# Kernel optimization log

Hardware: AMD Instinct MI355X
Metric: run time of the kernel (lower is better)

The kernel has to match this reference:

```python
import jax, jax.numpy as jnp
import numpy as np

B, S, H = 1, 2048, 4608
NH, NKV, HD = 36, 4, 128
GROUP = NH // NKV  # 9
ROPE_THETA = 100000.0
SLIDING_WINDOW = 1024


def _rope_tables(seq_len, head_dim):
    inv_freq = 1.0 / (ROPE_THETA ** (jnp.arange(0, head_dim, 2, dtype=jnp.float32) / head_dim))
    ang = jnp.arange(seq_len, dtype=jnp.float32)[:, None] * inv_freq[None, :]  # [S, HD/2]
    emb = jnp.concatenate([ang, ang], axis=-1)  # [S, HD]
    return jnp.cos(emb), jnp.sin(emb)


def setup_inputs() -> dict:
    key = jax.random.key(0)
    ks = jax.random.split(key, 10)
    std = 0.02
    cos_table, sin_table = _rope_tables(S, HD)
    return {
        "hidden_states": jax.random.normal(ks[0], (B, S, H), jnp.float32),
        "position_ids": jnp.broadcast_to(jnp.arange(S, dtype=jnp.int64)[None, :], (B, S)),
        "cos_table": cos_table,
        "sin_table": sin_table,
        "q_w": jax.random.normal(ks[1], (NH * HD, H), jnp.float32) * std,
        "q_b": jax.random.normal(ks[2], (NH * HD,), jnp.float32) * std,
        "k_w": jax.random.normal(ks[3], (NKV * HD, H), jnp.float32) * std,
        "k_b": jax.random.normal(ks[4], (NKV * HD,), jnp.float32) * std,
        "v_w": jax.random.normal(ks[5], (NKV * HD, H), jnp.float32) * std,
        "v_b": jax.random.normal(ks[6], (NKV * HD,), jnp.float32) * std,
        "o_w": jax.random.normal(ks[7], (H, NH * HD), jnp.float32) * std,
        "o_b": jax.random.normal(ks[8], (H,), jnp.float32) * std,
        "sliding_window": SLIDING_WINDOW,
    }


def _rotate_half(x):
    x1, x2 = jnp.split(x, 2, axis=-1)
    return jnp.concatenate([-x2, x1], axis=-1)


def reference(hidden_states, position_ids, cos_table, sin_table,
              q_w, q_b, k_w, k_b, v_w, v_b, o_w, o_b, sliding_window):
    bsz, q_len, _ = hidden_states.shape
    scaling = HD ** -0.5

    q = (hidden_states @ q_w.T + q_b).reshape(bsz, q_len, NH, HD)
    k = (hidden_states @ k_w.T + k_b).reshape(bsz, q_len, NKV, HD)
    v = (hidden_states @ v_w.T + v_b).reshape(bsz, q_len, NKV, HD)

    # RoPE with explicit cos/sin, unsqueeze_dim=2 ('bsnd' layout)
    cos = cos_table[position_ids][:, :, None, :]  # [B, S, 1, HD]
    sin = sin_table[position_ids][:, :, None, :]
    q = q * cos + _rotate_half(q) * sin
    k = k * cos + _rotate_half(k) * sin

    # GQA: group Q heads per KV head
    qg = q.reshape(bsz, q_len, NKV, GROUP, HD)
    logits = jnp.einsum('bqgrd,bkgd->bgrqk', qg, k) * scaling  # [B, NKV, GROUP, S, S]

    # causal + sliding-window mask: attend where k <= q and q - k < window
    idx = jnp.arange(q_len)
    mask = (idx[:, None] >= idx[None, :]) & (idx[:, None] - idx[None, :] < sliding_window)
    logits = jnp.where(mask[None, None, None, :, :], logits, jnp.finfo(logits.dtype).min)

    probs = jax.nn.softmax(logits, axis=-1)
    attn = jnp.einsum('bgrqk,bkgd->bqgrd', probs, v).reshape(bsz, q_len, NH * HD)
    return attn @ o_w.T + o_b
```

## Files before the change

kernel.cpp:

```cpp
#include <hip/hip_runtime.h>
#include <stdint.h>

typedef __attribute__((ext_vector_type(8))) __bf16 bf16x8;
typedef __attribute__((ext_vector_type(4))) float f32x4;
typedef __attribute__((ext_vector_type(8))) unsigned short u16x8;
typedef __attribute__((ext_vector_type(4))) unsigned short u16x4;

#define SEQ 2048
#define HID 4608
#define NQKV 5632
#define NHEAD 36
#define NKVH 4
#define HDIM 128
#define WINDOW 1024

__device__ __forceinline__ unsigned short f2b(float f) {
    unsigned u = __builtin_bit_cast(unsigned, f);
    u += 0x7fffu + ((u >> 16) & 1u);
    return (unsigned short)(u >> 16);
}
__device__ __forceinline__ float b2f(unsigned short h) {
    unsigned u = ((unsigned)h) << 16;
    return __builtin_bit_cast(float, u);
}

#define GLD16(gp, lp) __builtin_amdgcn_global_load_lds( \
    (const __attribute__((address_space(1))) void*)(gp), \
    (__attribute__((address_space(3))) void*)(lp), 16, 0, 0)

#define VMCNT8() asm volatile("s_waitcnt vmcnt(8)" ::: "memory")
#define VMCNT4() asm volatile("s_waitcnt vmcnt(4)" ::: "memory")
#define VMCNT0() asm volatile("s_waitcnt vmcnt(0)" ::: "memory")
#define BARRIER() asm volatile("s_barrier" ::: "memory")

__global__ __launch_bounds__(256) void conv_all_kernel(
    const float* __restrict__ s0, unsigned short* __restrict__ d0, int n0,
    const float* __restrict__ s1, unsigned short* __restrict__ d1, int n1,
    const float* __restrict__ s2, unsigned short* __restrict__ d2, int n2,
    const float* __restrict__ s3, unsigned short* __restrict__ d3, int n3,
    const float* __restrict__ s4, unsigned short* __restrict__ d4, int n4)
{
    int total = n0 + n1 + n2 + n3 + n4;
    int stride = gridDim.x * blockDim.x;
    for (int i = blockIdx.x * blockDim.x + threadIdx.x; i < total; i += stride) {
        const float* src; unsigned short* dst; int j = i;
        if (j < n0) { src = s0; dst = d0; }
        else if ((j -= n0) < n1) { src = s1; dst = d1; }
        else if ((j -= n1) < n2) { src = s2; dst = d2; }
        else if ((j -= n2) < n3) { src = s3; dst = d3; }
        else { j -= n3; src = s4; dst = d4; }
        float4 v = ((const float4*)src)[j];
        ushort4 o;
        o.x = f2b(v.x); o.y = f2b(v.y); o.z = f2b(v.z); o.w = f2b(v.w);
        ((ushort4*)dst)[j] = o;
    }
}

__global__ __launch_bounds__(512, 2) void gemm256_kernel(
    const unsigned short* __restrict__ A,
    const unsigned short* __restrict__ W,
    void* __restrict__ out,
    const float* __restrict__ b0, const float* __restrict__ b1, const float* __restrict__ b2,
    int N, int K, int GX, int outf32)
{
    __shared__ alignas(16) unsigned short ldsA[2][256 * 64];
    __shared__ alignas(16) unsigned short ldsB[2][256 * 64];

    const int tid = threadIdx.x;
    const int w = tid >> 6, lane = tid & 63;
    const int r16 = lane & 15, kg = lane >> 4;
    const int wm = w >> 2, wn = w & 3;

    const int cpx = gridDim.x >> 3;
    const int o = blockIdx.x;
    const int id = (o & 7) * cpx + (o >> 3);
    const int bx = id % GX, by = id / GX;
    const int row0 = by * 256, col0 = bx * 256;

    const int lr = lane >> 3;
    const int lc = lane & 7;
    const int cg = lc ^ lr;
    const unsigned short* Abase = A + (size_t)row0 * K;
    const unsigned short* Wbase = W + (size_t)col0 * K;

    auto STG = [&](const unsigned short* Mat, unsigned short* ldsSlot, int hf, int kb) {
#pragma unroll
        for (int j = 0; j < 2; ++j) {
            int row = hf * 128 + (w * 2 + j) * 8 + lr;
            GLD16(Mat + (size_t)row * K + kb + cg * 8,
                  (char*)ldsSlot + hf * 16384 + (w * 2 + j) * 1024);
        }
    };

    const int NITER = K >> 7;
    f32x4 acc[8][4] = {};
    const int swz = r16 & 7;

    bf16x8 af[4][2], bfA[2][2], bfB[2][2];

#define DSR_A(mh, Sl) \
_Pragma("unroll") for (int mi = 0; mi < 4; ++mi) \
_Pragma("unroll") for (int kh = 0; kh < 2; ++kh) \
    af[mi][kh] = *(const bf16x8*)((Sl) + (wm * 128 + (mh) * 64 + mi * 16 + r16) * 64 + ((kh * 4 + kg) ^ swz) * 8);
#define DSR_B(nh, Sl, BF) \
_Pragma("unroll") for (int ni = 0; ni < 2; ++ni) \
_Pragma("unroll") for (int kh = 0; kh < 2; ++kh) \
    BF[ni][kh] = *(const bf16x8*)((Sl) + (wn * 64 + (nh) * 32 + ni * 16 + r16) * 64 + ((kh * 4 + kg) ^ swz) * 8);
#define MFMA_Q(mh, nh, BF) \
    asm volatile("s_waitcnt lgkmcnt(0)" ::: "memory"); \
    __builtin_amdgcn_sched_barrier(0); \
    __builtin_amdgcn_s_setprio(1); \
_Pragma("unroll") for (int mi = 0; mi < 4; ++mi) \
_Pragma("unroll") for (int ni = 0; ni < 2; ++ni) \
_Pragma("unroll") for (int kh = 0; kh < 2; ++kh) \
    acc[(mh) * 4 + mi][(nh) * 2 + ni] = __builtin_amdgcn_mfma_f32_16x16x32_bf16(af[mi][kh], BF[ni][kh], acc[(mh) * 4 + mi][(nh) * 2 + ni], 0, 0, 0); \
    __builtin_amdgcn_s_setprio(0); \
    __builtin_amdgcn_sched_barrier(0);

    STG(Abase, ldsA[0], 0, 0);  STG(Abase, ldsA[0], 1, 0);
    STG(Wbase, ldsB[0], 0, 0);  STG(Wbase, ldsB[0], 1, 0);
    STG(Abase, ldsA[1], 0, 64); STG(Abase, ldsA[1], 1, 64);
    STG(Wbase, ldsB[1], 0, 64); STG(Wbase, ldsB[1], 1, 64);
    VMCNT0();
    BARRIER();

    for (int i = 0; i < NITER; ++i) {
        const unsigned short* A0 = ldsA[0];
        const unsigned short* B0 = ldsB[0];
        const unsigned short* A1 = ldsA[1];
        const unsigned short* B1 = ldsB[1];
        const bool st = (i + 1 < NITER);
        const int kb0 = (i + 1) * 128;
        const int kb1 = kb0 + 64;

        DSR_A(0, A0); DSR_B(0, B0, bfA);
        BARRIER();
        MFMA_Q(0, 0, bfA);
        BARRIER();
        DSR_B(1, B0, bfB);
        BARRIER();
        MFMA_Q(0, 1, bfB);
        BARRIER();
        DSR_A(1, A0);
        if (st) STG(Wbase, ldsB[0], 0, kb0);
        BARRIER();
        MFMA_Q(1, 1, bfB);
        BARRIER();
        if (st) { STG(Abase, ldsA[0], 0, kb0); VMCNT4(); } else { VMCNT0(); }
        BARRIER();
        MFMA_Q(1, 0, bfA);
        BARRIER();
        DSR_A(0, A1); DSR_B(0, B1, bfA);
        if (st) STG(Abase, ldsA[0], 1, kb0);
        BARRIER();
        MFMA_Q(0, 0, bfA);
        BARRIER();
        DSR_B(1, B1, bfB);
        if (st) STG(Wbase, ldsB[0], 1, kb0);
        BARRIER();
        MFMA_Q(0, 1, bfB);
        BARRIER();
        DSR_A(1, A1);
        if (st) { STG(Wbase, ldsB[1], 0, kb1); STG(Wbase, ldsB[1], 1, kb1); }
        BARRIER();
        MFMA_Q(1, 1, bfB);
        BARRIER();
        if (st) { STG(Abase, ldsA[1], 0, kb1); STG(Abase, ldsA[1], 1, kb1); VMCNT8(); }
        BARRIER();
        MFMA_Q(1, 0, bfA);
        BARRIER();
    }

    if (!outf32) {
        unsigned short* O = (unsigned short*)out;
#pragma unroll
        for (int m = 0; m < 8; ++m)
#pragma unroll
            for (int n = 0; n < 4; ++n)
#pragma unroll
                for (int r = 0; r < 4; ++r) {
                    int row = row0 + wm * 128 + m * 16 + kg * 4 + r;
                    int col = col0 + wn * 64 + n * 16 + r16;
                    float bias = (col < HID) ? b0[col]
                               : (col < HID + 512 ? b1[col - HID] : b2[col - HID - 512]);
                    O[(size_t)row * N + col] = f2b(acc[m][n][r] + bias);
                }
    } else {
        float* O = (float*)out;
#pragma unroll
        for (int m = 0; m < 8; ++m)
#pragma unroll
            for (int n = 0; n < 4; ++n)
#pragma unroll
                for (int r = 0; r < 4; ++r) {
                    int row = row0 + wm * 128 + m * 16 + kg * 4 + r;
                    int col = col0 + wn * 64 + n * 16 + r16;
                    O[(size_t)row * N + col] = acc[m][n][r] + b0[col];
                }
    }
#undef DSR_A
#undef DSR_B
#undef MFMA_Q
}

__global__ __launch_bounds__(256) void rope_kernel(unsigned short* __restrict__ qkv,
                                                   const float* __restrict__ cos_t,
                                                   const float* __restrict__ sin_t) {
    int idx = blockIdx.x * 256 + threadIdx.x;
    int d = idx & 63;
    int t = idx >> 6;
    int head = t % 40;
    int s = t / 40;
    int base = head < NHEAD ? head * HDIM : HID + (head - NHEAD) * HDIM;
    size_t off = (size_t)s * NQKV + base;
    float x = b2f(qkv[off + d]);
    float y = b2f(qkv[off + d + 64]);
    float c = cos_t[s * HDIM + d];
    float sn = sin_t[s * HDIM + d];
    qkv[off + d]      = f2b(x * c - y * sn);
    qkv[off + d + 64] = f2b(y * c + x * sn);
}

__global__ __launch_bounds__(256) void vtrans_kernel(const unsigned short* __restrict__ qkv,
                                                     unsigned short* __restrict__ vtg) {
    __shared__ unsigned short tile[32][36];
    const int s0 = blockIdx.x * 32, d0 = blockIdx.y * 32, kvh = blockIdx.z;
    const int lid = threadIdx.x;
    {
        int sl = lid >> 3, dc = (lid & 7) * 4;
        u16x4 v = *(const u16x4*)(qkv + (size_t)(s0 + sl) * NQKV + HID + 512 + kvh * HDIM + d0 + dc);
#pragma unroll
        for (int i = 0; i < 4; ++i) tile[sl][dc + i] = v[i];
    }
    __syncthreads();
    {
        int dl = lid >> 3, sc = (lid & 7) * 4;
        u16x4 v;
#pragma unroll
        for (int i = 0; i < 4; ++i) v[i] = tile[sc + i][dl];
        *(u16x4*)(vtg + (size_t)kvh * HDIM * SEQ + (size_t)(d0 + dl) * SEQ + s0 + sc) = v;
    }
}

#define KSTR 136
#define VSTR 72
#define PSTR 88
__global__ __launch_bounds__(256) void attn_kernel(const unsigned short* __restrict__ qkv,
                                                   const unsigned short* __restrict__ vtg,
                                                   unsigned short* __restrict__ aout)
{
    __shared__ alignas(16) unsigned short Ks[64 * KSTR];
    __shared__ alignas(16) unsigned short Vt[128 * VSTR];
    __shared__ alignas(16) unsigned short Ps[4 * 16 * PSTR];
    const int h = blockIdx.x, qb = blockIdx.y;
    const int q0 = qb * 64;
    const int kvh = h / 9;
    const int tid = threadIdx.x, wid = tid >> 6, lane = tid & 63;
    const int r16 = lane & 15, kg = lane >> 4;
    const int qbase = q0 + wid * 16;
    const unsigned short* vsrc = vtg + (size_t)kvh * HDIM * SEQ;

    bf16x8 qf[4];
    {
        const unsigned short* qrow = qkv + (size_t)(qbase + r16) * NQKV + h * HDIM;
#pragma unroll
        for (int kk = 0; kk < 4; ++kk)
            qf[kk] = *(const bf16x8*)(qrow + kk * 32 + kg * 8);
    }

    f32x4 o[8] = {};
    float mrow[4], lrow[4];
#pragma unroll
    for (int r = 0; r < 4; ++r) { mrow[r] = -1e30f; lrow[r] = 0.f; }

    int lo = q0 - (WINDOW - 1); if (lo < 0) lo = 0; lo &= ~63;
    unsigned short* myP = Ps + wid * 16 * PSTR;
    const float scale = 0.08838834764831845f;

    u16x8 kreg[4], vreg[4];
#define PREF(KT) \
_Pragma("unroll") for (int j = 0; j < 4; ++j) { \
        int c = tid + j * 256; \
        int key = c >> 4, dc = c & 15; \
        kreg[j] = *(const u16x8*)(qkv + (size_t)((KT) + key) * NQKV + HID + kvh * HDIM + dc * 8); \
        int d = c >> 3, k8 = (c & 7) * 8; \
        vreg[j] = *(const u16x8*)(vsrc + (size_t)d * SEQ + (KT) + k8); \
    }

    PREF(lo);

    for (int kt = lo; kt <= q0; kt += 64) {
#pragma unroll
        for (int j = 0; j < 4; ++j) {
            int c = tid + j * 256;
            int key = c >> 4, dc = c & 15;
            *(u16x8*)(Ks + key * KSTR + dc * 8) = kreg[j];
            int d = c >> 3, k8 = (c & 7) * 8;
            *(u16x8*)(Vt + d * VSTR + k8) = vreg[j];
        }
        __syncthreads();

        if (kt + 64 <= q0) { PREF(kt + 64); }

        f32x4 sc[4] = {};
#pragma unroll
        for (int t = 0; t < 4; ++t)
#pragma unroll
            for (int kk = 0; kk < 4; ++kk) {
                bf16x8 kf = *(const bf16x8*)(Ks + (t * 16 + r16) * KSTR + kk * 32 + kg * 8);
                sc[t] = __builtin_amdgcn_mfma_f32_16x16x32_bf16(qf[kk], kf, sc[t], 0, 0, 0);
            }

        float p[4][4], mt[4];
#pragma unroll
        for (int r = 0; r < 4; ++r) mt[r] = -1e30f;
#pragma unroll
        for (int t = 0; t < 4; ++t)
#pragma unroll
            for (int r = 0; r < 4; ++r) {
                int q = qbase + kg * 4 + r;
                int key = kt + t * 16 + r16;
                bool valid = (key <= q) && (q - key < WINDOW);
                float v = valid ? sc[t][r] * scale : -1e30f;
                p[t][r] = v;
                mt[r] = fmaxf(mt[r], v);
            }
#pragma unroll
        for (int mask = 1; mask <= 8; mask <<= 1)
#pragma unroll
            for (int r = 0; r < 4; ++r)
                mt[r] = fmaxf(mt[r], __shfl_xor(mt[r], mask, 64));

        float alpha[4], tsum[4];
#pragma unroll
        for (int r = 0; r < 4; ++r) {
            float mnew = fmaxf(mrow[r], mt[r]);
            alpha[r] = __expf(mrow[r] - mnew);
            mrow[r] = mnew;
            tsum[r] = 0.f;
        }
#pragma unroll
        for (int t = 0; t < 4; ++t)
#pragma unroll
            for (int r = 0; r < 4; ++r) {
                float e = __expf(p[t][r] - mrow[r]);
                p[t][r] = e;
                tsum[r] += e;
            }
#pragma unroll
        for (int mask = 1; mask <= 8; mask <<= 1)
#pragma unroll
            for (int r = 0; r < 4; ++r)
                tsum[r] += __shfl_xor(tsum[r], mask, 64);
#pragma unroll
        for (int r = 0; r < 4; ++r)
            lrow[r] = lrow[r] * alpha[r] + tsum[r];
#pragma unroll
        for (int n = 0; n < 8; ++n)
#pragma unroll
            for (int r = 0; r < 4; ++r)
                o[n][r] = o[n][r] * alpha[r];

#pragma unroll
        for (int t = 0; t < 4; ++t)
#pragma unroll
            for (int r = 0; r < 4; ++r)
                myP[(kg * 4 + r) * PSTR + t * 16 + r16] = f2b(p[t][r]);
        asm volatile("s_waitcnt lgkmcnt(0)" ::: "memory");

#pragma unroll
        for (int kc = 0; kc < 2; ++kc) {
            bf16x8 pa = *(const bf16x8*)(myP + r16 * PSTR + kc * 32 + kg * 8);
#pragma unroll
            for (int n = 0; n < 8; ++n) {
                bf16x8 vb = *(const bf16x8*)(Vt + (n * 16 + r16) * VSTR + kc * 32 + kg * 8);
                o[n] = __builtin_amdgcn_mfma_f32_16x16x32_bf16(pa, vb, o[n], 0, 0, 0);
            }
        }
        BARRIER();
    }
#undef PREF

#pragma unroll
    for (int n = 0; n < 8; ++n)
#pragma unroll
        for (int r = 0; r < 4; ++r) {
            int q = qbase + kg * 4 + r;
            aout[(size_t)q * HID + h * HDIM + n * 16 + r16] = f2b(o[n][r] / lrow[r]);
        }
}

extern "C" void kernel_launch(void* const* d_in, const int* in_sizes, int n_in,
                              void* d_out, int out_size, void* d_ws, size_t ws_size,
                              hipStream_t stream) {
    const float* hidden = (const float*)d_in[0];
    const float* cos_t = (const float*)d_in[2];
    const float* sin_t = (const float*)d_in[3];
    const float* q_w = (const float*)d_in[4];
    const float* q_b = (const float*)d_in[5];
    const float* k_w = (const float*)d_in[6];
    const float* k_b = (const float*)d_in[7];
    const float* v_w = (const float*)d_in[8];
    const float* v_b = (const float*)d_in[9];
    const float* o_w = (const float*)d_in[10];
    const float* o_b = (const float*)d_in[11];

    char* ws = (char*)d_ws;
    unsigned short* hbf  = (unsigned short*)ws;
    unsigned short* attn = hbf;
    unsigned short* wqkv = (unsigned short*)(ws + 18874368);
    unsigned short* vtg  = wqkv;
    unsigned short* wo   = (unsigned short*)(ws + 70778880);
    unsigned short* qkv  = (unsigned short*)(ws + 113246208);

    dim3 blk(256);
    conv_all_kernel<<<4096, blk, 0, stream>>>(
        hidden, hbf,                          (SEQ * HID) / 4,
        q_w,    wqkv,                         (HID * HID) / 4,
        k_w,    wqkv + (size_t)HID * HID,     (512 * HID) / 4,
        v_w,    wqkv + (size_t)5120 * HID,    (512 * HID) / 4,
        o_w,    wo,                           (HID * HID) / 4);

    gemm256_kernel<<<dim3(176), dim3(512), 0, stream>>>(hbf, wqkv, qkv, q_b, k_b, v_b, NQKV, HID, 22, 0);
    rope_kernel<<<(SEQ * 40 * 64) / 256, blk, 0, stream>>>(qkv, cos_t, sin_t);
    vtrans_kernel<<<dim3(SEQ / 32, HDIM / 32, NKVH), blk, 0, stream>>>(qkv, vtg);
    attn_kernel<<<dim3(NHEAD, SEQ / 64), blk, 0, stream>>>(qkv, vtg, attn);
    gemm256_kernel<<<dim3(144), dim3(512), 0, stream>>>(attn, wo, d_out, o_b, nullptr, nullptr, HID, HID, 18, 1);
}
```

Measured before the change: 433.0 us.

## Software-pipeline LDS fragment reads with MFMA in GEMM main loop

Restructures the 256x256 GEMM inner loop so LDS fragment reads for the next quarter-tile are issued before the current MFMA block, using double-buffered A fragments (afX/afY). The number of barriers per iteration drops from sixteen to eight, and global-to-LDS stage loads are re-sequenced to wait with vmcnt(2) instead of 4/8. The goal is to hide LDS latency behind matrix math and cut barrier stalls. The cost is extra registers for the second A fragment buffer under the 512-thread, 2-block launch bound, plus delicate ordering between LDS buffer reuse and barriers that could cause races. It also makes the wave index wave-uniform via readfirstlane.

```diff
diff --git a/kernel.cpp b/kernel.cpp
--- a/kernel.cpp
+++ b/kernel.cpp
@@ -28,9 +28,10 @@
     (const __attribute__((address_space(1))) void*)(gp), \
     (__attribute__((address_space(3))) void*)(lp), 16, 0, 0)
 
-#define VMCNT8() asm volatile("s_waitcnt vmcnt(8)" ::: "memory")
-#define VMCNT4() asm volatile("s_waitcnt vmcnt(4)" ::: "memory")
+#define VMCNT2() asm volatile("s_waitcnt vmcnt(2)" ::: "memory")
 #define VMCNT0() asm volatile("s_waitcnt vmcnt(0)" ::: "memory")
+#define LGKM0()  asm volatile("s_waitcnt lgkmcnt(0)" ::: "memory")
+#define SB0()    __builtin_amdgcn_sched_barrier(0)
 #define BARRIER() asm volatile("s_barrier" ::: "memory")
 
 __global__ __launch_bounds__(256) void conv_all_kernel(
@@ -67,7 +68,8 @@
     __shared__ alignas(16) unsigned short ldsB[2][256 * 64];
 
     const int tid = threadIdx.x;
-    const int w = tid >> 6, lane = tid & 63;
+    const int lane = tid & 63;
+    const int w  = __builtin_amdgcn_readfirstlane(tid >> 6);
     const int r16 = lane & 15, kg = lane >> 4;
     const int wm = w >> 2, wn = w & 3;
 
@@ -96,78 +98,83 @@
     f32x4 acc[8][4] = {};
     const int swz = r16 & 7;
 
-    bf16x8 af[4][2], bfA[2][2], bfB[2][2];
-
-#define DSR_A(mh, Sl) \
+    bf16x8 afX[4][2], afY[4][2], bfA[2][2], bfB[2][2];
+
+#define DSR_A(mh, Sl, AF) \
 _Pragma("unroll") for (int mi = 0; mi < 4; ++mi) \
 _Pragma("unroll") for (int kh = 0; kh < 2; ++kh) \
-    af[mi][kh] = *(const bf16x8*)((Sl) + (wm * 128 + (mh) * 64 + mi * 16 + r16) * 64 + ((kh * 4 + kg) ^ swz) * 8);
+    AF[mi][kh] = *(const bf16x8*)((Sl) + (wm * 128 + (mh) * 64 + mi * 16 + r16) * 64 + ((kh * 4 + kg) ^ swz) * 8);
 #define DSR_B(nh, Sl, BF) \
 _Pragma("unroll") for (int ni = 0; ni < 2; ++ni) \
 _Pragma("unroll") for (int kh = 0; kh < 2; ++kh) \
     BF[ni][kh] = *(const bf16x8*)((Sl) + (wn * 64 + (nh) * 32 + ni * 16 + r16) * 64 + ((kh * 4 + kg) ^ swz) * 8);
-#define MFMA_Q(mh, nh, BF) \
-    asm volatile("s_waitcnt lgkmcnt(0)" ::: "memory"); \
-    __builtin_amdgcn_sched_barrier(0); \
+#define MFMA_Q(mh, nh, AF, BF) \
+    SB0(); \
     __builtin_amdgcn_s_setprio(1); \
 _Pragma("unroll") for (int mi = 0; mi < 4; ++mi) \
 _Pragma("unroll") for (int ni = 0; ni < 2; ++ni) \
 _Pragma("unroll") for (int kh = 0; kh < 2; ++kh) \
-    acc[(mh) * 4 + mi][(nh) * 2 + ni] = __builtin_amdgcn_mfma_f32_16x16x32_bf16(af[mi][kh], BF[ni][kh], acc[(mh) * 4 + mi][(nh) * 2 + ni], 0, 0, 0); \
+    acc[(mh) * 4 + mi][(nh) * 2 + ni] = __builtin_amdgcn_mfma_f32_16x16x32_bf16(AF[mi][kh], BF[ni][kh], acc[(mh) * 4 + mi][(nh) * 2 + ni], 0, 0, 0); \
     __builtin_amdgcn_s_setprio(0); \
-    __builtin_amdgcn_sched_barrier(0);
+    SB0();
+
+    const unsigned short* A0 = ldsA[0];
+    const unsigned short* B0 = ldsB[0];
+    const unsigned short* A1 = ldsA[1];
+    const unsigned short* B1 = ldsB[1];
 
     STG(Abase, ldsA[0], 0, 0);  STG(Abase, ldsA[0], 1, 0);
     STG(Wbase, ldsB[0], 0, 0);  STG(Wbase, ldsB[0], 1, 0);
-    STG(Abase, ldsA[1], 0, 64); STG(Abase, ldsA[1], 1, 64);
+    STG(Abase, ldsA[1], 0, 64);
     STG(Wbase, ldsB[1], 0, 64); STG(Wbase, ldsB[1], 1, 64);
     VMCNT0();
     BARRIER();
+    DSR_A(0, A0, afX); DSR_B(0, B0, bfA);
 
     for (int i = 0; i < NITER; ++i) {
-        const unsigned short* A0 = ldsA[0];
-        const unsigned short* B0 = ldsB[0];
-        const unsigned short* A1 = ldsA[1];
-        const unsigned short* B1 = ldsB[1];
         const bool st = (i + 1 < NITER);
+        const int kbc1 = i * 128 + 64;
         const int kb0 = (i + 1) * 128;
         const int kb1 = kb0 + 64;
 
-        DSR_A(0, A0); DSR_B(0, B0, bfA);
-        BARRIER();
-        MFMA_Q(0, 0, bfA);
-        BARRIER();
+        LGKM0(); SB0();
         DSR_B(1, B0, bfB);
-        BARRIER();
-        MFMA_Q(0, 1, bfB);
-        BARRIER();
-        DSR_A(1, A0);
+        MFMA_Q(0, 0, afX, bfA);
+        STG(Abase, ldsA[1], 1, kbc1);
+        BARRIER();
+        LGKM0(); SB0();
+        DSR_A(1, A0, afY);
+        MFMA_Q(0, 1, afX, bfB);
         if (st) STG(Wbase, ldsB[0], 0, kb0);
         BARRIER();
-        MFMA_Q(1, 1, bfB);
-        BARRIER();
-        if (st) { STG(Abase, ldsA[0], 0, kb0); VMCNT4(); } else { VMCNT0(); }
-        BARRIER();
-        MFMA_Q(1, 0, bfA);
-        BARRIER();
-        DSR_A(0, A1); DSR_B(0, B1, bfA);
+        LGKM0(); SB0();
+        if (st) VMCNT2(); else VMCNT0();
+        DSR_A(0, A1, afX);
+        MFMA_Q(1, 1, afY, bfB);
+        if (st) { STG(Abase, ldsA[0], 0, kb0); STG(Wbase, ldsB[0], 1, kb0); }
+        BARRIER();
+        LGKM0(); SB0();
+        MFMA_Q(1, 0, afY, bfA);
+        DSR_B(0, B1, bfA);
+        BARRIER();
+        LGKM0(); SB0();
+        DSR_B(1, B1, bfB);
+        MFMA_Q(0, 0, afX, bfA);
         if (st) STG(Abase, ldsA[0], 1, kb0);
         BARRIER();
-        MFMA_Q(0, 0, bfA);
-        BARRIER();
-        DSR_B(1, B1, bfB);
-        if (st) STG(Wbase, ldsB[0], 1, kb0);
-        BARRIER();
-        MFMA_Q(0, 1, bfB);
-        BARRIER();
-        DSR_A(1, A1);
-        if (st) { STG(Wbase, ldsB[1], 0, kb1); STG(Wbase, ldsB[1], 1, kb1); }
-        BARRIER();
-        MFMA_Q(1, 1, bfB);
-        BARRIER();
-        if (st) { STG(Abase, ldsA[1], 0, kb1); STG(Abase, ldsA[1], 1, kb1); VMCNT8(); }
-        BARRIER();
-        MFMA_Q(1, 0, bfA);
+        LGKM0(); SB0();
+        DSR_A(1, A1, afY);
+        MFMA_Q(0, 1, afX, bfB);
+        if (st) STG(Wbase, ldsB[1], 0, kb1);
+        BARRIER();
+        LGKM0(); SB0();
+        if (st) { VMCNT2(); DSR_A(0, A0, afX); }
+        MFMA_Q(1, 1, afY, bfB);
+        if (st) { STG(Abase, ldsA[1], 0, kb1); STG(Wbase, ldsB[1], 1, kb1); }
+        BARRIER();
+        LGKM0(); SB0();
+        MFMA_Q(1, 0, afY, bfA);
+        if (st) DSR_B(0, B0, bfA);
         BARRIER();
     }
 
```

Result: faster. 422.4 us (-2.4%).

## Overlap o_w bf16 conversion with QKV GEMM using extra idle blocks

Applied to the files above, without the earlier changes.

Moves the fp32-to-bf16 conversion of the output projection weight out of the upfront conversion kernel and into 80 extra blocks appended to the QKV GEMM launch. The QKV GEMM uses 176 blocks, which leaves compute units idle on the 256-CU device, so the conversion can run on those free units at the same time as the GEMM. The GEMM block swizzle now uses the GEMM block count GB instead of gridDim. The risk is that the conversion's memory bandwidth competes with the GEMM's loads.

```diff
diff --git a/kernel.cpp b/kernel.cpp
--- a/kernel.cpp
+++ b/kernel.cpp
@@ -37,18 +37,16 @@
     const float* __restrict__ s0, unsigned short* __restrict__ d0, int n0,
     const float* __restrict__ s1, unsigned short* __restrict__ d1, int n1,
     const float* __restrict__ s2, unsigned short* __restrict__ d2, int n2,
-    const float* __restrict__ s3, unsigned short* __restrict__ d3, int n3,
-    const float* __restrict__ s4, unsigned short* __restrict__ d4, int n4)
+    const float* __restrict__ s3, unsigned short* __restrict__ d3, int n3)
 {
-    int total = n0 + n1 + n2 + n3 + n4;
+    int total = n0 + n1 + n2 + n3;
     int stride = gridDim.x * blockDim.x;
     for (int i = blockIdx.x * blockDim.x + threadIdx.x; i < total; i += stride) {
         const float* src; unsigned short* dst; int j = i;
         if (j < n0) { src = s0; dst = d0; }
         else if ((j -= n0) < n1) { src = s1; dst = d1; }
         else if ((j -= n1) < n2) { src = s2; dst = d2; }
-        else if ((j -= n2) < n3) { src = s3; dst = d3; }
-        else { j -= n3; src = s4; dst = d4; }
+        else { j -= n2; src = s3; dst = d3; }
         float4 v = ((const float4*)src)[j];
         ushort4 o;
         o.x = f2b(v.x); o.y = f2b(v.y); o.z = f2b(v.z); o.w = f2b(v.w);
@@ -61,18 +59,32 @@
     const unsigned short* __restrict__ W,
     void* __restrict__ out,
     const float* __restrict__ b0, const float* __restrict__ b1, const float* __restrict__ b2,
-    int N, int K, int GX, int outf32)
+    int N, int K, int GX, int GB, int outf32,
+    const float* __restrict__ cw_src, unsigned short* __restrict__ cw_dst, int cw_n4)
 {
+    const int tid = threadIdx.x;
+    const int o = blockIdx.x;
+
+    if (o >= GB) {
+        int cb = o - GB, ncb = gridDim.x - GB;
+        int stride = ncb * 512;
+        for (int i = cb * 512 + tid; i < cw_n4; i += stride) {
+            float4 v = ((const float4*)cw_src)[i];
+            ushort4 u;
+            u.x = f2b(v.x); u.y = f2b(v.y); u.z = f2b(v.z); u.w = f2b(v.w);
+            ((ushort4*)cw_dst)[i] = u;
+        }
+        return;
+    }
+
     __shared__ alignas(16) unsigned short ldsA[2][256 * 64];
     __shared__ alignas(16) unsigned short ldsB[2][256 * 64];
 
-    const int tid = threadIdx.x;
     const int w = tid >> 6, lane = tid & 63;
     const int r16 = lane & 15, kg = lane >> 4;
     const int wm = w >> 2, wn = w & 3;
 
-    const int cpx = gridDim.x >> 3;
-    const int o = blockIdx.x;
+    const int cpx = GB >> 3;
     const int id = (o & 7) * cpx + (o >> 3);
     const int bx = id % GX, by = id / GX;
     const int row0 = by * 256, col0 = bx * 256;
@@ -418,12 +430,15 @@
         hidden, hbf,                          (SEQ * HID) / 4,
         q_w,    wqkv,                         (HID * HID) / 4,
         k_w,    wqkv + (size_t)HID * HID,     (512 * HID) / 4,
-        v_w,    wqkv + (size_t)5120 * HID,    (512 * HID) / 4,
-        o_w,    wo,                           (HID * HID) / 4);
-
-    gemm256_kernel<<<dim3(176), dim3(512), 0, stream>>>(hbf, wqkv, qkv, q_b, k_b, v_b, NQKV, HID, 22, 0);
+        v_w,    wqkv + (size_t)5120 * HID,    (512 * HID) / 4);
+
+    gemm256_kernel<<<dim3(256), dim3(512), 0, stream>>>(
+        hbf, wqkv, qkv, q_b, k_b, v_b, NQKV, HID, 22, 176, 0,
+        o_w, wo, (HID * HID) / 4);
     rope_kernel<<<(SEQ * 40 * 64) / 256, blk, 0, stream>>>(qkv, cos_t, sin_t);
     vtrans_kernel<<<dim3(SEQ / 32, HDIM / 32, NKVH), blk, 0, stream>>>(qkv, vtg);
     attn_kernel<<<dim3(NHEAD, SEQ / 64), blk, 0, stream>>>(qkv, vtg, attn);
-    gemm256_kernel<<<dim3(144), dim3(512), 0, stream>>>(attn, wo, d_out, o_b, nullptr, nullptr, HID, HID, 18, 1);
-}
+    gemm256_kernel<<<dim3(144), dim3(512), 0, stream>>>(
+        attn, wo, d_out, o_b, nullptr, nullptr, HID, HID, 18, 144, 1,
+        nullptr, nullptr, 0);
+}
```

New measurement: 419.7 us. -3.1%, faster.
